# Kernel optimization log

Hardware: AMD Instinct MI355X
Metric: run time of the kernel (lower is better)

## Reference

```python
import jax, jax.numpy as jnp
import numpy as np

TEMPERATURE = 12.5
SINK_EPS = 0.05
SINK_ITERS = 100


def setup_inputs() -> dict:
    key = jax.random.key(0)
    k1, k2, k3, k4 = jax.random.split(key, 4)
    b, n_way, k_shot, q, c, h, w = 8, 5, 1, 75, 640, 7, 7
    return {
        "support_xf": jax.random.normal(k1, (b, n_way * k_shot, c, h, w), jnp.float32),
        "query_xf": jax.random.normal(k2, (b, q, c, h, w), jnp.float32),
        "support_y": jax.random.randint(k3, (b, n_way * k_shot), 0, n_way),
        "query_y": jax.random.randint(k4, (b, q), 0, n_way),
        "n_way": n_way,
        "k_shot": k_shot,
    }


def _sinkhorn_flow(cost, log_a, log_b, eps=SINK_EPS, iters=SINK_ITERS):
    """Entropic-OT (Sinkhorn, log-domain) replacement for cv2.EMD.
    cost: [..., m, n]; log_a: [..., m]; log_b: [..., n] (log of prob marginals).
    Returns transport plan P with row sums ~ exp(log_a), col sums ~ exp(log_b)."""
    f = jnp.zeros_like(log_a)
    g = jnp.zeros_like(log_b)

    def body(_, fg):
        f, g = fg
        f = eps * (log_a - jax.nn.logsumexp((g[..., None, :] - cost) / eps, axis=-1))
        g = eps * (log_b - jax.nn.logsumexp((f[..., :, None] - cost) / eps, axis=-2))
        return (f, g)

    f, g = jax.lax.fori_loop(0, iters, body, (f, g))
    return jnp.exp((f[..., :, None] + g[..., None, :] - cost) / eps)


def _deep_emd_logits(support, query):
    # support: [b, p, c, h, w] (1 prototype per class), query: [b, q, c, h, w]
    b, p, c, h, w = support.shape
    q = query.shape[1]
    hw = h * w
    sup = support.reshape(b, p, c, hw)
    qry = query.reshape(b, q, c, hw)

    # get_weight_vector: inner product of local features with the other set's GAP vector
    sup_gap = sup.mean(-1)  # [b, p, c]
    qry_gap = qry.mean(-1)  # [b, q, c]
    w1 = jax.nn.relu(jnp.einsum('bqcm,bpc->bqpm', qry, sup_gap)) + 1e-3  # [b,q,p,hw]
    w2 = jax.nn.relu(jnp.einsum('bpcn,bqc->bqpn', sup, qry_gap)) + 1e-3  # [b,q,p,hw] (weight_2[j,i] transposed)

    # normalize_feature: subtract per-image channel mean; then cosine similarity over channels
    supn = sup - sup.mean(2, keepdims=True)
    qryn = qry - qry.mean(2, keepdims=True)
    supn = supn / jnp.maximum(jnp.linalg.norm(supn, axis=2, keepdims=True), 1e-8)
    qryn = qryn / jnp.maximum(jnp.linalg.norm(qryn, axis=2, keepdims=True), 1e-8)
    S = jnp.einsum('bqcm,bpcn->bqpmn', qryn, supn)  # [b,q,p,hw,hw]

    # emd_inference marginal normalization: relu(w)+1e-5, rescaled so sum = hw -> prob = w/sum(w)
    wa = w1 + 1e-5
    wb = w2 + 1e-5
    log_a = jnp.log(wa) - jnp.log(wa.sum(-1, keepdims=True))
    log_b = jnp.log(wb) - jnp.log(wb.sum(-1, keepdims=True))

    flow = _sinkhorn_flow(1.0 - S, log_a, log_b) * hw  # total mass = hw as in cv2.EMD path
    flow = jax.lax.stop_gradient(flow)  # original flow comes from numpy -> constant

    logits = (S * flow).sum((-2, -1)) * (TEMPERATURE / hw)  # [b, q, p]
    return logits.reshape(b * q, p)


def reference(support_xf, query_xf, support_y, query_y, n_way, k_shot):
    # training / 1-shot path: pick first shot per class
    b = support_xf.shape[0]
    c, h, w = support_xf.shape[2:]
    sup = support_xf.reshape(b, n_way, k_shot, c, h, w)[:, :, 0]
    logits = _deep_emd_logits(sup, query_xf)  # [b*q, n_way]
    labels = query_y.reshape(-1)
    logp = jax.nn.log_softmax(logits, axis=-1)
    loss = -jnp.take_along_axis(logp, labels[:, None], axis=1).mean()
    return loss
```

## Files before the change

### kernel.cpp

```cpp
#include <hip/hip_runtime.h>
#include <math.h>

#define BB 8
#define PP 5
#define QQ 75
#define CC 640
#define HW 49
#define NIMG_Q (BB*QQ)
#define NIMG_S (BB*PP)
#define NPROB  (BB*QQ*PP)
#define TEMP 12.5f

#define CHUNKS 20
#define TROW 16
#define TCH  (HW*TROW)
#define TIMG (CHUNKS*TCH)
#define SROW 25
#define SPROB (HW*SROW)

#define OFF_SGAP   0
#define OFF_QGAP   (OFF_SGAP  + NIMG_S*CC)
#define OFF_SMEAN  (OFF_QGAP  + NIMG_Q*CC)
#define OFF_SINV   (OFF_SMEAN + NIMG_S*HW)
#define OFF_QMEAN  (OFF_SINV  + NIMG_S*HW)
#define OFF_QINV   (OFF_QMEAN + NIMG_Q*HW)
#define OFF_MARGA  (OFF_QINV  + NIMG_Q*HW)
#define OFF_MARGB  (OFF_MARGA + NPROB*HW)
#define OFF_QT     (OFF_MARGB + NPROB*HW)
#define OFF_ST     (OFF_QT    + NIMG_Q*TIMG)
#define OFF_S16    (OFF_ST    + NIMG_S*TIMG)
#define OFF_LOGITS (OFF_S16   + NPROB*SPROB)

typedef _Float16 f16x8 __attribute__((ext_vector_type(8)));
typedef float f32x4 __attribute__((ext_vector_type(4)));
#define MFMAH __builtin_amdgcn_mfma_f32_16x16x32_f16

__device__ __forceinline__ float wsum64(float v) {
#pragma unroll
    for (int off = 32; off > 0; off >>= 1) v += __shfl_xor(v, off, 64);
    return v;
}
__device__ __forceinline__ float rlf(float x, int l) {
    return __int_as_float(__builtin_amdgcn_readlane(__float_as_int(x), l));
}
__device__ __forceinline__ unsigned packh2(float a, float b) {
    union { _Float16 h[2]; unsigned u; } pk;
    pk.h[0] = (_Float16)a; pk.h[1] = (_Float16)b;
    return pk.u;
}
__device__ __forceinline__ float f16lo(unsigned w) {
    union { unsigned short s; _Float16 h; } u; u.s = (unsigned short)w; return (float)u.h;
}
__device__ __forceinline__ float f16hi(unsigned w) {
    union { unsigned short s; _Float16 h; } u; u.s = (unsigned short)(w >> 16); return (float)u.h;
}

__global__ __launch_bounds__(256) void sgap_kernel(const float* __restrict__ sup,
                                                   float* __restrict__ ws) {
    int img = blockIdx.x;
    int tid = threadIdx.x;
    const float* X = sup + (size_t)img * CC * HW;
    float* gap = ws + OFF_SGAP + img * CC;
    for (int c = tid; c < CC; c += 256) {
        const float* row = X + c * HW;
        float s = 0.f;
#pragma unroll
        for (int g = 0; g < 6; g++) {
            float rv[8];
#pragma unroll
            for (int j = 0; j < 8; j++) rv[j] = row[g * 8 + j];
#pragma unroll
            for (int j = 0; j < 8; j++) s += rv[j];
        }
        s += row[48];
        gap[c] = s * (1.0f / HW);
    }
}

__global__ __launch_bounds__(512) __attribute__((amdgpu_waves_per_eu(4, 4)))
void prep_kernel(const float* __restrict__ sup, const float* __restrict__ qry,
                 float* __restrict__ ws) {
    int g = blockIdx.x;
    int tid = threadIdx.x;
    int lane = tid & 63;
    int wv = tid >> 6;

    __shared__ float XSG[PP * CC];
    __shared__ float cs_p[8][52], sq_p[8][52];
    __shared__ float part[8][PP][52];
    __shared__ float muL[52], invL[52];

    if (g < 600) {
        int img = g;
        int b = img / QQ;
        const float* X = qry + (size_t)img * CC * HW;
        const float* sg = ws + OFF_SGAP + b * PP * CC;
        float* gap = ws + OFF_QGAP + img * CC;

        for (int i = tid; i < PP * CC / 4; i += 512)
            ((float4*)XSG)[i] = ((const float4*)sg)[i];
        __syncthreads();

        float cs = 0.f, sq = 0.f;
        float acc[PP] = {0.f, 0.f, 0.f, 0.f, 0.f};
        if (lane < HW) {
            for (int c8 = wv * 80; c8 < wv * 80 + 80; c8 += 16) {
                float v[16];
#pragma unroll
                for (int j = 0; j < 16; j++) v[j] = X[(c8 + j) * HW + lane];
#pragma unroll
                for (int j = 0; j < 16; j++) {
                    cs += v[j];
                    sq = fmaf(v[j], v[j], sq);
                }
#pragma unroll
                for (int p = 0; p < PP; p++) {
                    float a = acc[p];
#pragma unroll
                    for (int qv = 0; qv < 4; qv++) {
                        float4 g0 = *(const float4*)&XSG[p * CC + c8 + 4 * qv];
                        a = fmaf(v[4 * qv + 0], g0.x, a);
                        a = fmaf(v[4 * qv + 1], g0.y, a);
                        a = fmaf(v[4 * qv + 2], g0.z, a);
                        a = fmaf(v[4 * qv + 3], g0.w, a);
                    }
                    acc[p] = a;
                }
            }
        }
        if (lane < 52) {
            cs_p[wv][lane] = (lane < HW) ? cs : 0.f;
            sq_p[wv][lane] = (lane < HW) ? sq : 0.f;
#pragma unroll
            for (int p = 0; p < PP; p++) part[wv][p][lane] = (lane < HW) ? acc[p] : 0.f;
        }
        __syncthreads();
        if (wv == 0) {
            if (lane < HW) {
                float c4 = 0.f, s4 = 0.f;
#pragma unroll
                for (int w = 0; w < 8; w++) { c4 += cs_p[w][lane]; s4 += sq_p[w][lane]; }
                float mu = c4 * (1.0f / CC);
                float nsq = fmaxf(s4 - c4 * c4 * (1.0f / CC), 0.f);
                float inv = 1.0f / fmaxf(sqrtf(nsq), 1e-8f);
                ws[OFF_QMEAN + img * HW + lane] = mu;
                ws[OFF_QINV + img * HW + lane] = inv;
                muL[lane] = mu;
                invL[lane] = inv;
            }
#pragma unroll
            for (int p = 0; p < PP; p++) {
                float a = 0.f;
                if (lane < 52) {
#pragma unroll
                    for (int w = 0; w < 8; w++) a += part[w][p][lane];
                }
                float w = (lane < HW) ? (fmaxf(a, 0.f) + 1.01e-3f) : 0.f;
                float s = wsum64(w);
                if (lane < HW) ws[OFF_MARGA + (img * PP + p) * HW + lane] = w / s;
            }
        }
        for (int c = tid; c < CC; c += 512) {
            const float* row = X + c * HW;
            float s = 0.f;
#pragma unroll
            for (int gg = 0; gg < 6; gg++) {
                float rv[8];
#pragma unroll
                for (int j = 0; j < 8; j++) rv[j] = row[gg * 8 + j];
#pragma unroll
                for (int j = 0; j < 8; j++) s += rv[j];
            }
            s += row[48];
            gap[c] = s * (1.0f / HW);
        }
        __syncthreads();
        unsigned* T = (unsigned*)ws + OFF_QT + (size_t)img * TIMG;
        int m = lane;
        if (m < HW) {
            float mu = muL[m], inv = invL[m];
            for (int t = wv; t < CHUNKS; t += 8) {
                float va[32];
#pragma unroll
                for (int j = 0; j < 32; j++) va[j] = X[(t * 32 + j) * HW + m];
                unsigned pk[16];
#pragma unroll
                for (int w = 0; w < 16; w++)
                    pk[w] = packh2((va[2 * w] - mu) * inv, (va[2 * w + 1] - mu) * inv);
                uint4* dst = (uint4*)(T + t * TCH + m * TROW);
#pragma unroll
                for (int u = 0; u < 4; u++)
                    dst[u] = make_uint4(pk[4 * u], pk[4 * u + 1], pk[4 * u + 2], pk[4 * u + 3]);
            }
        }
    } else {
        int img = g - 600;
        const float* X = sup + (size_t)img * CC * HW;

        float cs = 0.f, sq = 0.f;
        if (lane < HW) {
            for (int c8 = wv * 80; c8 < wv * 80 + 80; c8 += 8) {
                float v[8];
#pragma unroll
                for (int j = 0; j < 8; j++) v[j] = X[(c8 + j) * HW + lane];
#pragma unroll
                for (int j = 0; j < 8; j++) {
                    cs += v[j];
                    sq = fmaf(v[j], v[j], sq);
                }
            }
        }
        if (lane < 52) {
            cs_p[wv][lane] = (lane < HW) ? cs : 0.f;
            sq_p[wv][lane] = (lane < HW) ? sq : 0.f;
        }
        __syncthreads();
        if (wv == 0 && lane < HW) {
            float c4 = 0.f, s4 = 0.f;
#pragma unroll
            for (int w = 0; w < 8; w++) { c4 += cs_p[w][lane]; s4 += sq_p[w][lane]; }
            float mu = c4 * (1.0f / CC);
            float nsq = fmaxf(s4 - c4 * c4 * (1.0f / CC), 0.f);
            float inv = 1.0f / fmaxf(sqrtf(nsq), 1e-8f);
            ws[OFF_SMEAN + img * HW + lane] = mu;
            ws[OFF_SINV + img * HW + lane] = inv;
            muL[lane] = mu;
            invL[lane] = inv;
        }
        __syncthreads();
        unsigned* T = (unsigned*)ws + OFF_ST + (size_t)img * TIMG;
        int m = lane;
        if (m < HW) {
            float mu = muL[m], inv = invL[m];
            for (int t = wv; t < CHUNKS; t += 8) {
                float va[32];
#pragma unroll
                for (int j = 0; j < 32; j++) va[j] = X[(t * 32 + j) * HW + m];
                unsigned pk[16];
#pragma unroll
                for (int w = 0; w < 16; w++)
                    pk[w] = packh2((va[2 * w] - mu) * inv, (va[2 * w + 1] - mu) * inv);
                uint4* dst = (uint4*)(T + t * TCH + m * TROW);
#pragma unroll
                for (int u = 0; u < 4; u++)
                    dst[u] = make_uint4(pk[4 * u], pk[4 * u + 1], pk[4 * u + 2], pk[4 * u + 3]);
            }
        }
    }
}

__global__ __launch_bounds__(256, 2) void mgemm_kernel(const float* __restrict__ sup,
                                                       float* __restrict__ ws) {
    __shared__ unsigned LDSU[CHUNKS * TCH];

    int g = blockIdx.x;
    int tid = threadIdx.x;
    int lane = tid & 63;
    int wv = tid >> 6;

    if (g < 600) {
        int xcd = g & 7;
        int k = g >> 3;
        int p = k % 5;
        int gidx = xcd + 8 * (k / 5);
        int b = gidx / 15;
        int qg = gidx - b * 15;
        int lrow = lane & 15;
        int quad = lane >> 4;

        const unsigned* Bt = (const unsigned*)ws + OFF_ST + (size_t)(b * PP + p) * TIMG;
        for (int idx = tid; idx < CHUNKS * HW * 4; idx += 256) {
            int r = idx >> 2;
            int q = idx & 3;
            int t = r / 49;
            int n = r - t * 49;
            uint4 v = *(const uint4*)(Bt + (idx << 2));
            *(uint4*)(&LDSU[t * TCH + n * 16 + ((q ^ ((n >> 1) & 3)) << 2)]) = v;
        }
        __syncthreads();

        int bof[4];
#pragma unroll
        for (int nt = 0; nt < 4; nt++) {
            int n = 16 * nt + lrow;
            if (n > 48) n = 48;
            bof[nt] = n * 16 + ((quad ^ ((n >> 1) & 3)) << 2);
        }

        const unsigned* Aq = (const unsigned*)ws + OFF_QT + (size_t)(b * QQ + qg * 5) * TIMG;
        int arow = (16 * wv + lrow) * TROW + quad * 4;

        f32x4 acc[5][4];
#pragma unroll
        for (int qi = 0; qi < 5; qi++)
#pragma unroll
            for (int nt = 0; nt < 4; nt++) acc[qi][nt] = (f32x4){0.f, 0.f, 0.f, 0.f};

#pragma unroll 2
        for (int t = 0; t < CHUNKS; t++) {
            f16x8 bfr[4];
#pragma unroll
            for (int nt = 0; nt < 4; nt++)
                bfr[nt] = *(const f16x8*)(&LDSU[t * TCH + bof[nt]]);
#pragma unroll
            for (int qi = 0; qi < 5; qi++) {
                f16x8 a = *(const f16x8*)(Aq + (size_t)qi * TIMG + t * TCH + arow);
#pragma unroll
                for (int nt = 0; nt < 4; nt++)
                    acc[qi][nt] = MFMAH(a, bfr[nt], acc[qi][nt], 0, 0, 0);
            }
        }

        __syncthreads();
        float* S_lds = (float*)LDSU;
#pragma unroll
        for (int qi = 0; qi < 5; qi++)
#pragma unroll
            for (int nt = 0; nt < 4; nt++)
#pragma unroll
                for (int r = 0; r < 4; r++) {
                    int mm = 16 * wv + quad * 4 + r;
                    int nn = 16 * nt + lrow;
                    if (mm < HW && nn < HW) S_lds[qi * 2597 + mm * 53 + nn] = acc[qi][nt][r];
                }
        __syncthreads();

        for (int qi = 0; qi < 5; qi++) {
            int prob = (b * QQ + qg * 5 + qi) * PP + p;
            unsigned* Sp = (unsigned*)ws + OFF_S16 + (size_t)prob * SPROB;
            const float* Sl = S_lds + qi * 2597;
            for (int idx = tid; idx < SPROB; idx += 256) {
                int row = idx / SROW;
                int w = idx - row * SROW;
                int n0 = 2 * w;
                float v0 = Sl[row * 53 + n0];
                float v1 = (n0 + 1 < HW) ? Sl[row * 53 + n0 + 1] : 0.f;
                Sp[idx] = packh2(v0, v1);
            }
        }
    } else {
        int id = g - 600;
        int qc = id % 5;
        int bp = id / 5;
        int b = bp / PP;
        int p = bp % PP;
        const float* X = sup + (size_t)bp * CC * HW;
        const float* qg = ws + OFF_QGAP + (b * QQ + qc * 15) * CC;

        float* QG = (float*)LDSU;
        float (*part)[15][52] = (float (*)[15][52])((float*)LDSU + 15 * CC);
        for (int i = tid; i < 15 * CC / 4; i += 256)
            ((float4*)QG)[i] = ((const float4*)qg)[i];
        __syncthreads();

        float acc[15];
#pragma unroll
        for (int i = 0; i < 15; i++) acc[i] = 0.f;
        if (lane < HW) {
            for (int c8 = wv * 160; c8 < wv * 160 + 160; c8 += 8) {
                float sv[8];
#pragma unroll
                for (int j = 0; j < 8; j++) sv[j] = X[(c8 + j) * HW + lane];
#pragma unroll
                for (int qq = 0; qq < 15; qq++) {
                    float4 g0 = *(const float4*)&QG[qq * CC + c8];
                    float4 g1 = *(const float4*)&QG[qq * CC + c8 + 4];
                    float a = acc[qq];
                    a = fmaf(sv[0], g0.x, a); a = fmaf(sv[1], g0.y, a);
                    a = fmaf(sv[2], g0.z, a); a = fmaf(sv[3], g0.w, a);
                    a = fmaf(sv[4], g1.x, a); a = fmaf(sv[5], g1.y, a);
                    a = fmaf(sv[6], g1.z, a); a = fmaf(sv[7], g1.w, a);
                    acc[qq] = a;
                }
            }
        }
        __syncthreads();
        if (lane < 52) {
#pragma unroll
            for (int qq = 0; qq < 15; qq++) part[wv][qq][lane] = (lane < HW) ? acc[qq] : 0.f;
        }
        __syncthreads();
        if (wv == 0) {
#pragma unroll
            for (int qq = 0; qq < 15; qq++) {
                float a = 0.f;
                if (lane < 52)
                    a = part[0][qq][lane] + part[1][qq][lane] + part[2][qq][lane] + part[3][qq][lane];
                int q = qc * 15 + qq;
                float w = (lane < HW) ? (fmaxf(a, 0.f) + 1.01e-3f) : 0.f;
                float s = wsum64(w);
                if (lane < HW) ws[OFF_MARGB + ((b * QQ + q) * PP + p) * HW + lane] = w / s;
            }
        }
    }
}

#define FOR12(M) M(0) M(1) M(2) M(3) M(4) M(5) M(6) M(7) M(8) M(9) M(10) M(11)
#define KEXPF(s) __expf(fmaf(20.f, (s), -20.f))

__global__ __launch_bounds__(64)
__attribute__((amdgpu_waves_per_eu(3, 3)))
void sinkhorn_kernel(float* __restrict__ ws) {
    int prob = blockIdx.x;
    int lane = threadIdx.x;
    const unsigned* Sp = (const unsigned*)ws + OFF_S16 + (size_t)prob * SPROB;

    float am = 0.f, bm = 0.f;
    if (lane < HW) {
        am = ws[OFF_MARGA + prob * HW + lane];
        bm = ws[OFF_MARGB + prob * HW + lane];
    }
    int ll = (lane < HW) ? lane : 48;
    const unsigned* rbase = Sp + ll * SROW;
    int wof = ll >> 1;
    int sh = (ll & 1) * 16;

    float4 kr0, kr1, kr2, kr3, kr4, kr5, kr6, kr7, kr8, kr9, kr10, kr11;
    float4 kt0, kt1, kt2, kt3, kt4, kt5, kt6, kt7, kt8, kt9, kt10, kt11;
    float kr12x, kt12x;
#define KIR(g) { unsigned w0 = rbase[2*(g)]; unsigned w1 = rbase[2*(g)+1];  \
    kr##g = make_float4(KEXPF(f16lo(w0)), KEXPF(f16hi(w0)),                 \
                        KEXPF(f16lo(w1)), KEXPF(f16hi(w1))); }
    FOR12(KIR)
#undef KIR
    kr12x = KEXPF(f16lo(rbase[24]));
#define KIT(g) { \
    float s0 = f16lo((Sp[(4*(g)+0)*SROW + wof] >> sh) & 0xFFFFu);           \
    float s1 = f16lo((Sp[(4*(g)+1)*SROW + wof] >> sh) & 0xFFFFu);           \
    float s2 = f16lo((Sp[(4*(g)+2)*SROW + wof] >> sh) & 0xFFFFu);           \
    float s3 = f16lo((Sp[(4*(g)+3)*SROW + wof] >> sh) & 0xFFFFu);           \
    kt##g = make_float4(KEXPF(s0), KEXPF(s1), KEXPF(s2), KEXPF(s3)); }
    FOR12(KIT)
#undef KIT
    kt12x = KEXPF(f16lo((Sp[48 * SROW + wof] >> sh) & 0xFFFFu));

    float vv = (lane < HW) ? 1.f : 0.f;
    float uu = 0.f;

#pragma unroll 1
    for (int it = 0; it < 48; it++) {
        float t0 = 0.f, t1 = 0.f, t2 = 0.f, t3 = 0.f;
#define RS(g) { t0 = fmaf(kr##g.x, rlf(vv, 4*(g)+0), t0);                   \
                t1 = fmaf(kr##g.y, rlf(vv, 4*(g)+1), t1);                   \
                t2 = fmaf(kr##g.z, rlf(vv, 4*(g)+2), t2);                   \
                t3 = fmaf(kr##g.w, rlf(vv, 4*(g)+3), t3); }
        FOR12(RS)
#undef RS
        t0 = fmaf(kr12x, rlf(vv, 48), t0);
        float t = (t0 + t1) + (t2 + t3);
        uu = am * __builtin_amdgcn_rcpf(t);

        float s0 = 0.f, s1 = 0.f, s2 = 0.f, s3 = 0.f;
#define CS(g) { s0 = fmaf(kt##g.x, rlf(uu, 4*(g)+0), s0);                   \
                s1 = fmaf(kt##g.y, rlf(uu, 4*(g)+1), s1);                   \
                s2 = fmaf(kt##g.z, rlf(uu, 4*(g)+2), s2);                   \
                s3 = fmaf(kt##g.w, rlf(uu, 4*(g)+3), s3); }
        FOR12(CS)
#undef CS
        s0 = fmaf(kt12x, rlf(uu, 48), s0);
        float s = (s0 + s1) + (s2 + s3);
        vv = bm * __builtin_amdgcn_rcpf(s);
    }

    float ssum = 0.f;
#define FS(g) {                                                             \
    ssum = fmaf(kr##g.x * fmaf(0.05f, __logf(kr##g.x), 1.f), rlf(vv, 4*(g)+0), ssum); \
    ssum = fmaf(kr##g.y * fmaf(0.05f, __logf(kr##g.y), 1.f), rlf(vv, 4*(g)+1), ssum); \
    ssum = fmaf(kr##g.z * fmaf(0.05f, __logf(kr##g.z), 1.f), rlf(vv, 4*(g)+2), ssum); \
    ssum = fmaf(kr##g.w * fmaf(0.05f, __logf(kr##g.w), 1.f), rlf(vv, 4*(g)+3), ssum); }
    FOR12(FS)
#undef FS
    ssum = fmaf(kr12x * fmaf(0.05f, __logf(kr12x), 1.f), rlf(vv, 48), ssum);
    float contrib = (lane < HW) ? (uu * ssum) : 0.f;
    float tot = wsum64(contrib);
    if (lane == 0) ws[OFF_LOGITS + prob] = TEMP * tot;
}

__global__ __launch_bounds__(640) void loss_kernel(const float* __restrict__ ws,
                                                   const int* __restrict__ qy,
                                                   float* __restrict__ out) {
    int tid = threadIdx.x;
    float val = 0.f;
    if (tid < NIMG_Q) {
        const float* lg = ws + OFF_LOGITS + tid * PP;
        float l[PP];
        float mx = -1e30f;
#pragma unroll
        for (int p = 0; p < PP; p++) {
            l[p] = lg[p];
            mx = fmaxf(mx, l[p]);
        }
        float se = 0.f;
#pragma unroll
        for (int p = 0; p < PP; p++) se += __expf(l[p] - mx);
        float lse = mx + logf(se);
        int lab = qy[tid];
        val = -(l[lab] - lse);
    }
    __shared__ float red[16];
    float s = wsum64(val);
    if ((tid & 63) == 0) red[tid >> 6] = s;
    __syncthreads();
    if (tid == 0) {
        float tot = 0.f;
#pragma unroll
        for (int w = 0; w < 10; w++) tot += red[w];
        out[0] = tot * (1.0f / NIMG_Q);
    }
}

extern "C" void kernel_launch(void* const* d_in, const int* in_sizes, int n_in,
                              void* d_out, int out_size, void* d_ws, size_t ws_size,
                              hipStream_t stream) {
    const float* sup = (const float*)d_in[0];
    const float* qry = (const float*)d_in[1];
    const int* qy = (const int*)d_in[3];
    float* ws = (float*)d_ws;
    float* out = (float*)d_out;

    sgap_kernel<<<NIMG_S, 256, 0, stream>>>(sup, ws);
    prep_kernel<<<640, 512, 0, stream>>>(sup, qry, ws);
    mgemm_kernel<<<800, 256, 0, stream>>>(sup, ws);
    sinkhorn_kernel<<<NPROB, 64, 0, stream>>>(ws);
    loss_kernel<<<1, 640, 0, stream>>>(ws, qy, out);
}
```

Baseline: 258.4 us.

## Fuse MFMA similarity GEMM with Sinkhorn and regroup GAP/marginal kernels

The similarity GEMM and the Sinkhorn iterations now run in one 320-thread kernel. Four waves compute the 5 query-by-support S tiles with MFMA into LDS, then each of the five waves runs Sinkhorn for one problem, reading S straight from LDS. This removes the fp16 S write and re-read through global memory and one kernel launch. Query GAP moves into the GAP kernel and the marginal-B computation moves into the prep kernel, so dependencies are met without a separate mgemm stage. The tradeoff is that Sinkhorn now runs at 600 blocks of 5 waves with large LDS, down from 3000 independent single-wave blocks, which may lower occupancy and latency hiding.

```diff
diff --git a/kernel.cpp b/kernel.cpp
--- a/kernel.cpp
+++ b/kernel.cpp
@@ -48,19 +48,23 @@
     pk.h[0] = (_Float16)a; pk.h[1] = (_Float16)b;
     return pk.u;
 }
-__device__ __forceinline__ float f16lo(unsigned w) {
-    union { unsigned short s; _Float16 h; } u; u.s = (unsigned short)w; return (float)u.h;
-}
-__device__ __forceinline__ float f16hi(unsigned w) {
-    union { unsigned short s; _Float16 h; } u; u.s = (unsigned short)(w >> 16); return (float)u.h;
-}
-
-__global__ __launch_bounds__(256) void sgap_kernel(const float* __restrict__ sup,
-                                                   float* __restrict__ ws) {
+__device__ __forceinline__ float f16r(float x) { return (float)(_Float16)x; }
+
+__global__ __launch_bounds__(256) void gap_kernel(const float* __restrict__ sup,
+                                                  const float* __restrict__ qry,
+                                                  float* __restrict__ ws) {
     int img = blockIdx.x;
     int tid = threadIdx.x;
-    const float* X = sup + (size_t)img * CC * HW;
-    float* gap = ws + OFF_SGAP + img * CC;
+    const float* X;
+    float* gap;
+    if (img < NIMG_S) {
+        X = sup + (size_t)img * CC * HW;
+        gap = ws + OFF_SGAP + img * CC;
+    } else {
+        int q = img - NIMG_S;
+        X = qry + (size_t)q * CC * HW;
+        gap = ws + OFF_QGAP + q * CC;
+    }
     for (int c = tid; c < CC; c += 256) {
         const float* row = X + c * HW;
         float s = 0.f;
@@ -85,17 +89,20 @@
     int lane = tid & 63;
     int wv = tid >> 6;
 
-    __shared__ float XSG[PP * CC];
-    __shared__ float cs_p[8][52], sq_p[8][52];
-    __shared__ float part[8][PP][52];
-    __shared__ float muL[52], invL[52];
+    __shared__ float SH[12720];
 
     if (g < 600) {
+        float* XSG = SH;
+        float (*cs_p)[52] = (float (*)[52])(SH + 3200);
+        float (*sq_p)[52] = (float (*)[52])(SH + 3616);
+        float (*part)[PP][52] = (float (*)[PP][52])(SH + 4032);
+        float* muL = SH + 6112;
+        float* invL = SH + 6164;
+
         int img = g;
         int b = img / QQ;
         const float* X = qry + (size_t)img * CC * HW;
         const float* sg = ws + OFF_SGAP + b * PP * CC;
-        float* gap = ws + OFF_QGAP + img * CC;
 
         for (int i = tid; i < PP * CC / 4; i += 512)
             ((float4*)XSG)[i] = ((const float4*)sg)[i];
@@ -160,20 +167,6 @@
                 if (lane < HW) ws[OFF_MARGA + (img * PP + p) * HW + lane] = w / s;
             }
         }
-        for (int c = tid; c < CC; c += 512) {
-            const float* row = X + c * HW;
-            float s = 0.f;
-#pragma unroll
-            for (int gg = 0; gg < 6; gg++) {
-                float rv[8];
-#pragma unroll
-                for (int j = 0; j < 8; j++) rv[j] = row[gg * 8 + j];
-#pragma unroll
-                for (int j = 0; j < 8; j++) s += rv[j];
-            }
-            s += row[48];
-            gap[c] = s * (1.0f / HW);
-        }
         __syncthreads();
         unsigned* T = (unsigned*)ws + OFF_QT + (size_t)img * TIMG;
         int m = lane;
@@ -193,7 +186,12 @@
                     dst[u] = make_uint4(pk[4 * u], pk[4 * u + 1], pk[4 * u + 2], pk[4 * u + 3]);
             }
         }
-    } else {
+    } else if (g < 640) {
+        float (*cs_p)[52] = (float (*)[52])(SH + 3200);
+        float (*sq_p)[52] = (float (*)[52])(SH + 3616);
+        float* muL = SH + 6112;
+        float* invL = SH + 6164;
+
         int img = g - 600;
         const float* X = sup + (size_t)img * CC * HW;
 
@@ -246,100 +244,8 @@
                     dst[u] = make_uint4(pk[4 * u], pk[4 * u + 1], pk[4 * u + 2], pk[4 * u + 3]);
             }
         }
-    }
-}
-
-__global__ __launch_bounds__(256, 2) void mgemm_kernel(const float* __restrict__ sup,
-                                                       float* __restrict__ ws) {
-    __shared__ unsigned LDSU[CHUNKS * TCH];
-
-    int g = blockIdx.x;
-    int tid = threadIdx.x;
-    int lane = tid & 63;
-    int wv = tid >> 6;
-
-    if (g < 600) {
-        int xcd = g & 7;
-        int k = g >> 3;
-        int p = k % 5;
-        int gidx = xcd + 8 * (k / 5);
-        int b = gidx / 15;
-        int qg = gidx - b * 15;
-        int lrow = lane & 15;
-        int quad = lane >> 4;
-
-        const unsigned* Bt = (const unsigned*)ws + OFF_ST + (size_t)(b * PP + p) * TIMG;
-        for (int idx = tid; idx < CHUNKS * HW * 4; idx += 256) {
-            int r = idx >> 2;
-            int q = idx & 3;
-            int t = r / 49;
-            int n = r - t * 49;
-            uint4 v = *(const uint4*)(Bt + (idx << 2));
-            *(uint4*)(&LDSU[t * TCH + n * 16 + ((q ^ ((n >> 1) & 3)) << 2)]) = v;
-        }
-        __syncthreads();
-
-        int bof[4];
-#pragma unroll
-        for (int nt = 0; nt < 4; nt++) {
-            int n = 16 * nt + lrow;
-            if (n > 48) n = 48;
-            bof[nt] = n * 16 + ((quad ^ ((n >> 1) & 3)) << 2);
-        }
-
-        const unsigned* Aq = (const unsigned*)ws + OFF_QT + (size_t)(b * QQ + qg * 5) * TIMG;
-        int arow = (16 * wv + lrow) * TROW + quad * 4;
-
-        f32x4 acc[5][4];
-#pragma unroll
-        for (int qi = 0; qi < 5; qi++)
-#pragma unroll
-            for (int nt = 0; nt < 4; nt++) acc[qi][nt] = (f32x4){0.f, 0.f, 0.f, 0.f};
-
-#pragma unroll 2
-        for (int t = 0; t < CHUNKS; t++) {
-            f16x8 bfr[4];
-#pragma unroll
-            for (int nt = 0; nt < 4; nt++)
-                bfr[nt] = *(const f16x8*)(&LDSU[t * TCH + bof[nt]]);
-#pragma unroll
-            for (int qi = 0; qi < 5; qi++) {
-                f16x8 a = *(const f16x8*)(Aq + (size_t)qi * TIMG + t * TCH + arow);
-#pragma unroll
-                for (int nt = 0; nt < 4; nt++)
-                    acc[qi][nt] = MFMAH(a, bfr[nt], acc[qi][nt], 0, 0, 0);
-            }
-        }
-
-        __syncthreads();
-        float* S_lds = (float*)LDSU;
-#pragma unroll
-        for (int qi = 0; qi < 5; qi++)
-#pragma unroll
-            for (int nt = 0; nt < 4; nt++)
-#pragma unroll
-                for (int r = 0; r < 4; r++) {
-                    int mm = 16 * wv + quad * 4 + r;
-                    int nn = 16 * nt + lrow;
-                    if (mm < HW && nn < HW) S_lds[qi * 2597 + mm * 53 + nn] = acc[qi][nt][r];
-                }
-        __syncthreads();
-
-        for (int qi = 0; qi < 5; qi++) {
-            int prob = (b * QQ + qg * 5 + qi) * PP + p;
-            unsigned* Sp = (unsigned*)ws + OFF_S16 + (size_t)prob * SPROB;
-            const float* Sl = S_lds + qi * 2597;
-            for (int idx = tid; idx < SPROB; idx += 256) {
-                int row = idx / SROW;
-                int w = idx - row * SROW;
-                int n0 = 2 * w;
-                float v0 = Sl[row * 53 + n0];
-                float v1 = (n0 + 1 < HW) ? Sl[row * 53 + n0 + 1] : 0.f;
-                Sp[idx] = packh2(v0, v1);
-            }
-        }
     } else {
-        int id = g - 600;
+        int id = g - 640;
         int qc = id % 5;
         int bp = id / 5;
         int b = bp / PP;
@@ -347,16 +253,16 @@
         const float* X = sup + (size_t)bp * CC * HW;
         const float* qg = ws + OFF_QGAP + (b * QQ + qc * 15) * CC;
 
-        float* QG = (float*)LDSU;
-        float (*part)[15][52] = (float (*)[15][52])((float*)LDSU + 15 * CC);
-        for (int i = tid; i < 15 * CC / 4; i += 256)
+        float* QG = SH;
+        float (*part)[15][52] = (float (*)[15][52])(SH + 9600);
+        for (int i = tid; i < 15 * CC / 4; i += 512)
             ((float4*)QG)[i] = ((const float4*)qg)[i];
         __syncthreads();
 
         float acc[15];
 #pragma unroll
         for (int i = 0; i < 15; i++) acc[i] = 0.f;
-        if (lane < HW) {
+        if (wv < 4 && lane < HW) {
             for (int c8 = wv * 160; c8 < wv * 160 + 160; c8 += 8) {
                 float sv[8];
 #pragma unroll
@@ -375,7 +281,7 @@
             }
         }
         __syncthreads();
-        if (lane < 52) {
+        if (wv < 4 && lane < 52) {
 #pragma unroll
             for (int qq = 0; qq < 15; qq++) part[wv][qq][lane] = (lane < HW) ? acc[qq] : 0.f;
         }
@@ -398,12 +304,83 @@
 #define FOR12(M) M(0) M(1) M(2) M(3) M(4) M(5) M(6) M(7) M(8) M(9) M(10) M(11)
 #define KEXPF(s) __expf(fmaf(20.f, (s), -20.f))
 
-__global__ __launch_bounds__(64)
-__attribute__((amdgpu_waves_per_eu(3, 3)))
-void sinkhorn_kernel(float* __restrict__ ws) {
-    int prob = blockIdx.x;
-    int lane = threadIdx.x;
-    const unsigned* Sp = (const unsigned*)ws + OFF_S16 + (size_t)prob * SPROB;
+__global__ __launch_bounds__(320, 2) void fused_kernel(float* __restrict__ ws) {
+    __shared__ unsigned LDSU[CHUNKS * TCH];
+
+    int g = blockIdx.x;
+    int xcd = g & 7;
+    int k = g >> 3;
+    int p = k % 5;
+    int gidx = xcd + 8 * (k / 5);
+    int b = gidx / 15;
+    int qg = gidx - b * 15;
+
+    int tid = threadIdx.x;
+    int lane = tid & 63;
+    int wv = tid >> 6;
+    int lrow = lane & 15;
+    int quad = lane >> 4;
+
+    const unsigned* Bt = (const unsigned*)ws + OFF_ST + (size_t)(b * PP + p) * TIMG;
+    for (int idx = tid; idx < CHUNKS * HW * 4; idx += 320) {
+        int r = idx >> 2;
+        int q = idx & 3;
+        int t = r / 49;
+        int n = r - t * 49;
+        uint4 v = *(const uint4*)(Bt + (idx << 2));
+        *(uint4*)(&LDSU[t * TCH + n * 16 + ((q ^ ((n >> 1) & 3)) << 2)]) = v;
+    }
+    __syncthreads();
+
+    f32x4 acc[5][4];
+    if (wv < 4) {
+        int bof[4];
+#pragma unroll
+        for (int nt = 0; nt < 4; nt++) {
+            int n = 16 * nt + lrow;
+            if (n > 48) n = 48;
+            bof[nt] = n * 16 + ((quad ^ ((n >> 1) & 3)) << 2);
+        }
+        const unsigned* Aq = (const unsigned*)ws + OFF_QT + (size_t)(b * QQ + qg * 5) * TIMG;
+        int arow = (16 * wv + lrow) * TROW + quad * 4;
+#pragma unroll
+        for (int qi = 0; qi < 5; qi++)
+#pragma unroll
+            for (int nt = 0; nt < 4; nt++) acc[qi][nt] = (f32x4){0.f, 0.f, 0.f, 0.f};
+#pragma unroll 2
+        for (int t = 0; t < CHUNKS; t++) {
+            f16x8 bfr[4];
+#pragma unroll
+            for (int nt = 0; nt < 4; nt++)
+                bfr[nt] = *(const f16x8*)(&LDSU[t * TCH + bof[nt]]);
+#pragma unroll
+            for (int qi = 0; qi < 5; qi++) {
+                f16x8 a = *(const f16x8*)(Aq + (size_t)qi * TIMG + t * TCH + arow);
+#pragma unroll
+                for (int nt = 0; nt < 4; nt++)
+                    acc[qi][nt] = MFMAH(a, bfr[nt], acc[qi][nt], 0, 0, 0);
+            }
+        }
+    }
+    __syncthreads();
+    float* S_lds = (float*)LDSU;
+    if (wv < 4) {
+#pragma unroll
+        for (int qi = 0; qi < 5; qi++)
+#pragma unroll
+            for (int nt = 0; nt < 4; nt++)
+#pragma unroll
+                for (int r = 0; r < 4; r++) {
+                    int mm = 16 * wv + quad * 4 + r;
+                    int nn = 16 * nt + lrow;
+                    if (mm < HW && nn < HW) S_lds[qi * 2597 + mm * 53 + nn] = acc[qi][nt][r];
+                }
+    }
+    __syncthreads();
+
+    int qi = wv;
+    int prob = (b * QQ + qg * 5 + qi) * PP + p;
+    const float* Sq = S_lds + qi * 2597;
 
     float am = 0.f, bm = 0.f;
     if (lane < HW) {
@@ -411,28 +388,21 @@
         bm = ws[OFF_MARGB + prob * HW + lane];
     }
     int ll = (lane < HW) ? lane : 48;
-    const unsigned* rbase = Sp + ll * SROW;
-    int wof = ll >> 1;
-    int sh = (ll & 1) * 16;
+    const float* Srow = Sq + ll * 53;
 
     float4 kr0, kr1, kr2, kr3, kr4, kr5, kr6, kr7, kr8, kr9, kr10, kr11;
     float4 kt0, kt1, kt2, kt3, kt4, kt5, kt6, kt7, kt8, kt9, kt10, kt11;
     float kr12x, kt12x;
-#define KIR(g) { unsigned w0 = rbase[2*(g)]; unsigned w1 = rbase[2*(g)+1];  \
-    kr##g = make_float4(KEXPF(f16lo(w0)), KEXPF(f16hi(w0)),                 \
-                        KEXPF(f16lo(w1)), KEXPF(f16hi(w1))); }
+#define KIR(g) kr##g = make_float4(KEXPF(f16r(Srow[4*(g)+0])), KEXPF(f16r(Srow[4*(g)+1])), \
+                                   KEXPF(f16r(Srow[4*(g)+2])), KEXPF(f16r(Srow[4*(g)+3])));
     FOR12(KIR)
 #undef KIR
-    kr12x = KEXPF(f16lo(rbase[24]));
-#define KIT(g) { \
-    float s0 = f16lo((Sp[(4*(g)+0)*SROW + wof] >> sh) & 0xFFFFu);           \
-    float s1 = f16lo((Sp[(4*(g)+1)*SROW + wof] >> sh) & 0xFFFFu);           \
-    float s2 = f16lo((Sp[(4*(g)+2)*SROW + wof] >> sh) & 0xFFFFu);           \
-    float s3 = f16lo((Sp[(4*(g)+3)*SROW + wof] >> sh) & 0xFFFFu);           \
-    kt##g = make_float4(KEXPF(s0), KEXPF(s1), KEXPF(s2), KEXPF(s3)); }
+    kr12x = KEXPF(f16r(Srow[48]));
+#define KIT(g) kt##g = make_float4(KEXPF(f16r(Sq[(4*(g)+0)*53 + ll])), KEXPF(f16r(Sq[(4*(g)+1)*53 + ll])), \
+                                   KEXPF(f16r(Sq[(4*(g)+2)*53 + ll])), KEXPF(f16r(Sq[(4*(g)+3)*53 + ll])));
     FOR12(KIT)
 #undef KIT
-    kt12x = KEXPF(f16lo((Sp[48 * SROW + wof] >> sh) & 0xFFFFu));
+    kt12x = KEXPF(f16r(Sq[48 * 53 + ll]));
 
     float vv = (lane < HW) ? 1.f : 0.f;
     float uu = 0.f;
@@ -518,9 +488,8 @@
     float* ws = (float*)d_ws;
     float* out = (float*)d_out;
 
-    sgap_kernel<<<NIMG_S, 256, 0, stream>>>(sup, ws);
-    prep_kernel<<<640, 512, 0, stream>>>(sup, qry, ws);
-    mgemm_kernel<<<800, 256, 0, stream>>>(sup, ws);
-    sinkhorn_kernel<<<NPROB, 64, 0, stream>>>(ws);
+    gap_kernel<<<640, 256, 0, stream>>>(sup, qry, ws);
+    prep_kernel<<<840, 512, 0, stream>>>(sup, qry, ws);
+    fused_kernel<<<600, 320, 0, stream>>>(ws);
     loss_kernel<<<1, 640, 0, stream>>>(ws, qy, out);
 }
```

After: 302.8 us. +17.2%, slower.
